# Optimization experiments

Measured on AMD Instinct MI355X. Metric: run time of the kernel, lower is better.

Reference implementation:

```python
import jax, jax.numpy as jnp
import numpy as np

B, N, D, H, O = 8, 2048, 64, 64, 64
ALPHA = 2.0  # LeakyReLU negative slope per module default
NEG = -9e15


def _lin(x, W, b):
    # torch nn.Linear: y = x @ W.T + b, W is [out, in]
    return x @ W.T + b


def setup_inputs() -> dict:
    key = jax.random.key(0)
    ks = jax.random.split(key, 32)
    f32 = jnp.float32
    x = jax.random.normal(ks[0], (B, N, D), f32)
    adj = jax.random.randint(ks[1], (B, N, N), 0, 2).astype(f32)
    c = jax.random.normal(ks[2], (B, N, H), f32)
    h = jax.random.normal(ks[3], (B, N, H), f32)
    s = 0.1
    W = jax.random.normal(ks[4], (D, H), f32) * s           # GAT weight
    a = jax.random.normal(ks[5], (2 * H, 1), f32) * s       # GAT attention vector
    def lin(k, out_d, in_d):
        k1, k2 = jax.random.split(k)
        return (jax.random.normal(k1, (out_d, in_d), f32) * s,
                jax.random.normal(k2, (out_d,), f32) * s)
    Wf, bWf = lin(ks[6], H, H); Wi, bWi = lin(ks[7], H, H)
    Wo, bWo = lin(ks[8], H, H); Wc, bWc = lin(ks[9], H, H)
    Uf, bUf = lin(ks[10], H, D); Ui, bUi = lin(ks[11], H, D)
    Uo, bUo = lin(ks[12], H, D); Uc, bUc = lin(ks[13], H, D)
    Wout, bout = lin(ks[14], O, 2 * H)
    return dict(x=x, adj=adj, c=c, h=h, W=W, a=a,
                Wf=Wf, bWf=bWf, Wi=Wi, bWi=bWi, Wo=Wo, bWo=bWo, Wc=Wc, bWc=bWc,
                Uf=Uf, bUf=bUf, Ui=Ui, bUi=bUi, Uo=Uo, bUo=bUo, Uc=Uc, bUc=bUc,
                Wout=Wout, bout=bout)


def reference(x, adj, c, h, W, a,
              Wf, bWf, Wi, bWi, Wo, bWo, Wc, bWc,
              Uf, bUf, Ui, bUi, Uo, bUo, Uc, bUc,
              Wout, bout):
    # ---- GraphAttentionLayer (eval mode: dropout is identity) ----
    Wh = x @ W                                   # [B,N,H]
    # e[b,i,j] = leakyrelu(a[:H].Wh_i + a[H:].Wh_j) -- same math as the
    a_src = (Wh @ a[:H]).squeeze(-1)             # [B,N]
    a_dst = (Wh @ a[H:]).squeeze(-1)             # [B,N]
    e = jax.nn.leaky_relu(a_src[:, :, None] + a_dst[:, None, :], ALPHA)  # [B,N,N]
    att = jnp.where(adj > 0, e, NEG)
    att = jax.nn.softmax(att, axis=2)
    x_hidden = jax.nn.elu(att @ Wh)              # [B,N,H] (concat=True)
    # ---- LSTMLayer step ----
    f_t = jax.nn.sigmoid(_lin(h, Wf, bWf) + _lin(x, Uf, bUf))
    i_t = jax.nn.sigmoid(_lin(h, Wi, bWi) + _lin(x, Ui, bUi))
    o_t = jax.nn.sigmoid(_lin(h, Wo, bWo) + _lin(x, Uo, bUo))
    c_hat = jnp.tanh(_lin(h, Wc, bWc) + _lin(x, Uc, bUc))
    c_t = f_t * c + i_t * c_hat
    h_t = o_t * jax.nn.relu(c_t)                 # gate = nn.ReLU() default
    total = jnp.concatenate([x_hidden, h_t], axis=2)  # [B,N,2H]
    output = jax.nn.relu(_lin(total, Wout, bout))     # [B,N,O]
    return (output, h_t, c_t)
```

## Files before the change

### kernel.cpp

```cpp
#include <hip/hip_runtime.h>
#include <math.h>

#define B_ 8
#define N_ 2048
#define NT_ (B_*N_)
#define OUTSZ (NT_*64)

#define WS_ASRC  0
#define WS_ADST  (WS_ASRC + NT_)
#define WS_WT    (WS_ADST + NT_)
#define WS_BB    (WS_WT + 128*256)
#define WS_WOT   (WS_BB + 256)
#define WS_PD    (WS_WOT + 128*64)
#define WS_PN    (WS_PD + 8*NT_)

typedef float f32x4 __attribute__((ext_vector_type(4)));
typedef __bf16 bf16x8 __attribute__((ext_vector_type(8)));
typedef __bf16 bf16x4 __attribute__((ext_vector_type(4)));

__device__ __forceinline__ float lrelu2(float x) { return x > 0.f ? x : 2.f * x; }
__device__ __forceinline__ float f4get(const float4& v, int k) { return k==0?v.x:(k==1?v.y:(k==2?v.z:v.w)); }

__global__ __launch_bounds__(256) void k1_wh(const float* __restrict__ x, const float* __restrict__ W,
                                             const float* __restrict__ a, float* __restrict__ ws,
                                             __bf16* __restrict__ whT,
                                             const float* Wf, const float* Wi, const float* Wo, const float* Wc,
                                             const float* Uf, const float* Ui, const float* Uo, const float* Uc,
                                             const float* bWf, const float* bWi, const float* bWo, const float* bWc,
                                             const float* bUf, const float* bUi, const float* bUo, const float* bUc,
                                             const float* Wout)
{
    __shared__ float xl[64 * 68];
    __shared__ float Wl[64 * 68];
    int t = threadIdx.x;
    if (blockIdx.x >= 256) {
        int idx = (blockIdx.x - 256) * 256 + t;
        if (idx < 128 * 256) {
            int k = idx >> 8, o = idx & 255;
            int g = o >> 6, u = o & 63;
            const float* Wg = (g == 0) ? Wf : (g == 1) ? Wi : (g == 2) ? Wo : Wc;
            const float* Ug = (g == 0) ? Uf : (g == 1) ? Ui : (g == 2) ? Uo : Uc;
            ws[WS_WT + idx] = (k < 64) ? Wg[u * 64 + k] : Ug[u * 64 + (k - 64)];
        } else if (idx < 128 * 256 + 256) {
            int o = idx - 128 * 256;
            int g = o >> 6, u = o & 63;
            const float* bW = (g == 0) ? bWf : (g == 1) ? bWi : (g == 2) ? bWo : bWc;
            const float* bU = (g == 0) ? bUf : (g == 1) ? bUi : (g == 2) ? bUo : bUc;
            ws[WS_BB + o] = bW[u] + bU[u];
        } else if (idx < 128 * 256 + 256 + 128 * 64) {
            int j = idx - (128 * 256 + 256);
            int k = j >> 6, u = j & 63;
            ws[WS_WOT + j] = Wout[u * 128 + k];
        }
        return;
    }
    int i0 = blockIdx.x * 64;
    #pragma unroll
    for (int it = 0; it < 4; ++it) {
        int f = t + 256 * it;
        int r = f >> 4, q = f & 15;
        *(float4*)&xl[r * 68 + q * 4] = *(const float4*)&x[i0 * 64 + f * 4];
        *(float4*)&Wl[r * 68 + q * 4] = *(const float4*)&W[f * 4];
    }
    __syncthreads();
    int cg = t & 15, rg = t >> 4;
    int c0 = cg * 4, r0 = rg * 4;
    float acc[4][4] = {};
    #pragma unroll
    for (int d0 = 0; d0 < 64; d0 += 4) {
        float4 wv[4], xv[4];
        #pragma unroll
        for (int k = 0; k < 4; ++k) wv[k] = *(float4*)&Wl[(d0 + k) * 68 + c0];
        #pragma unroll
        for (int ri = 0; ri < 4; ++ri) xv[ri] = *(float4*)&xl[(r0 + ri) * 68 + d0];
        #pragma unroll
        for (int ri = 0; ri < 4; ++ri)
            #pragma unroll
            for (int k = 0; k < 4; ++k) {
                float xs = f4get(xv[ri], k);
                acc[ri][0] += xs * wv[k].x; acc[ri][1] += xs * wv[k].y;
                acc[ri][2] += xs * wv[k].z; acc[ri][3] += xs * wv[k].w;
            }
    }
    int b = i0 >> 11;
    int rowb0 = (i0 & 2047) + r0;
    #pragma unroll
    for (int cj = 0; cj < 4; ++cj) {
        bf16x4 v;
        v[0] = (__bf16)acc[0][cj]; v[1] = (__bf16)acc[1][cj];
        v[2] = (__bf16)acc[2][cj]; v[3] = (__bf16)acc[3][cj];
        *(bf16x4*)&whT[((size_t)(b * 64 + c0 + cj)) * N_ + rowb0] = v;
    }
    float4 a0 = *(const float4*)&a[c0];
    float4 a1 = *(const float4*)&a[64 + c0];
    #pragma unroll
    for (int ri = 0; ri < 4; ++ri) {
        int row = i0 + r0 + ri;
        float s0 = acc[ri][0]*a0.x + acc[ri][1]*a0.y + acc[ri][2]*a0.z + acc[ri][3]*a0.w;
        float s1 = acc[ri][0]*a1.x + acc[ri][1]*a1.y + acc[ri][2]*a1.z + acc[ri][3]*a1.w;
        #pragma unroll
        for (int m = 1; m < 16; m <<= 1) { s0 += __shfl_xor(s0, m, 64); s1 += __shfl_xor(s1, m, 64); }
        if (cg == 0) { ws[WS_ASRC + row] = s0; ws[WS_ADST + row] = s1; }
    }
}

__global__ __launch_bounds__(256) void k2v10(const float* __restrict__ adj,
                                             const __bf16* __restrict__ whT,
                                             float* __restrict__ ws)
{
    __shared__ __bf16 adjt[2][16][268];
    __shared__ float lsa[4][16][68];
    __shared__ float lsd[4][16];
    __shared__ float gred[4];
    int tid = threadIdx.x;
    int lane = tid & 63, w = tid >> 6;
    int r = lane & 15, g = lane >> 4;
    int jr = blockIdx.x & 7;
    int rslab = blockIdx.x >> 3;
    int b = rslab >> 4;
    int row_base = rslab * 128;
    int jbeg = jr * 256 + w * 64;

    {
        float gm = -3.0e38f;
        for (int i = tid; i < N_; i += 256) gm = fmaxf(gm, ws[WS_ADST + b * N_ + i]);
        #pragma unroll
        for (int m_ = 1; m_ < 64; m_ <<= 1) gm = fmaxf(gm, __shfl_xor(gm, m_, 64));
        if (lane == 0) gred[w] = gm;
    }
    __syncthreads();
    float gmax = fmaxf(fmaxf(gred[0], gred[1]), fmaxf(gred[2], gred[3]));

    bf16x8 bfr[2][4];
    #pragma unroll
    for (int ks = 0; ks < 2; ++ks)
        #pragma unroll
        for (int n = 0; n < 4; ++n)
            bfr[ks][n] = *(const bf16x8*)&whT[(size_t)(b * 64 + n * 16 + r) * N_ + jbeg + ks * 32 + g * 8];
    float ejr[2][8];
    #pragma unroll
    for (int ks = 0; ks < 2; ++ks) {
        float4 d0 = *(const float4*)&ws[WS_ADST + b * N_ + jbeg + ks * 32 + g * 8];
        float4 d1 = *(const float4*)&ws[WS_ADST + b * N_ + jbeg + ks * 32 + g * 8 + 4];
        ejr[ks][0]=__expf(d0.x); ejr[ks][1]=__expf(d0.y); ejr[ks][2]=__expf(d0.z); ejr[ks][3]=__expf(d0.w);
        ejr[ks][4]=__expf(d1.x); ejr[ks][5]=__expf(d1.y); ejr[ks][6]=__expf(d1.z); ejr[ks][7]=__expf(d1.w);
    }
    float asv8[8];
    #pragma unroll
    for (int tt = 0; tt < 8; ++tt)
        asv8[tt] = ws[WS_ASRC + row_base + tt * 16 + r];

    f32x4 sreg[2][4];

#define SLOAD(T, S)                                                                        \
    {                                                                                      \
        _Pragma("unroll")                                                                  \
        for (int i = 0; i < 4; ++i)                                                        \
            sreg[S][i] = *(const f32x4*)&adj[(size_t)(row_base + (T) * 16 + w * 4 + i) * N_ \
                                             + jr * 256 + lane * 4];                       \
    }
#define SWRITE(T, S)                                                                       \
    {                                                                                      \
        _Pragma("unroll")                                                                  \
        for (int i = 0; i < 4; ++i) {                                                      \
            bf16x4 bv;                                                                     \
            bv[0] = (__bf16)sreg[S][i][0]; bv[1] = (__bf16)sreg[S][i][1];                  \
            bv[2] = (__bf16)sreg[S][i][2]; bv[3] = (__bf16)sreg[S][i][3];                  \
            *(bf16x4*)&adjt[(T) & 1][w * 4 + i][lane * 4] = bv;                            \
        }                                                                                  \
    }

    SLOAD(0, 0);
    SWRITE(0, 0);
    SLOAD(1, 1);
    asm volatile("s_waitcnt lgkmcnt(0)" ::: "memory");
    __builtin_amdgcn_s_barrier();
    asm volatile("" ::: "memory");

    #pragma unroll
    for (int t = 0; t < 8; ++t) {
        const int s = t & 1;
        if (t + 2 < 8) { SLOAD(t + 2, s); }
        float as = asv8[t];
        float M  = lrelu2(as + gmax);
        float c1 = __expf(as - M);
        float c2 = __expf(2.f * as - M);
        float thr = __expf(-as);
        f32x4 acc[4] = {{0.f,0.f,0.f,0.f},{0.f,0.f,0.f,0.f},{0.f,0.f,0.f,0.f},{0.f,0.f,0.f,0.f}};
        float dsum = 0.f;
        #pragma unroll
        for (int ks = 0; ks < 2; ++ks) {
            bf16x8 at = *(const bf16x8*)&adjt[s][r][w * 64 + ks * 32 + g * 8];
            bf16x8 af;
            float ds_ = 0.f;
            #pragma unroll
            for (int e = 0; e < 8; ++e) {
                float avv = (float)at[e];
                float E = ejr[ks][e];
                float p = (E > thr) ? c1 * E : (c2 * E) * E;
                p = (avv > 0.f) ? p : 0.f;
                ds_ += p;
                af[e] = (__bf16)p;
            }
            dsum += ds_;
            #pragma unroll
            for (int n = 0; n < 4; ++n)
                acc[n] = __builtin_amdgcn_mfma_f32_16x16x32_bf16(af, bfr[ks][n], acc[n], 0, 0, 0);
        }
        dsum += __shfl_xor(dsum, 16, 64);
        dsum += __shfl_xor(dsum, 32, 64);
        #pragma unroll
        for (int n = 0; n < 4; ++n)
            #pragma unroll
            for (int i = 0; i < 4; ++i)
                lsa[w][g * 4 + i][n * 16 + r] = acc[n][i];
        if (g == 0) lsd[w][r] = dsum;
        if (t + 1 < 8) { SWRITE(t + 1, s ^ 1); }
        asm volatile("s_waitcnt lgkmcnt(0)" ::: "memory");
        __builtin_amdgcn_s_barrier();
        asm volatile("" ::: "memory");
        {
            int rl = tid >> 4, h0 = (tid & 15) * 4;
            float4 sv = make_float4(0.f, 0.f, 0.f, 0.f);
            #pragma unroll
            for (int w2 = 0; w2 < 4; ++w2) {
                float4 q = *(const float4*)&lsa[w2][rl][h0];
                sv.x += q.x; sv.y += q.y; sv.z += q.z; sv.w += q.w;
            }
            int row0 = row_base + t * 16;
            *(float4*)&ws[WS_PN + ((size_t)jr * NT_ + row0 + rl) * 64 + h0] = sv;
            if (tid < 16)
                ws[WS_PD + jr * NT_ + row0 + tid] =
                    lsd[0][tid] + lsd[1][tid] + lsd[2][tid] + lsd[3][tid];
        }
        asm volatile("s_waitcnt lgkmcnt(0)" ::: "memory");
        __builtin_amdgcn_s_barrier();
        asm volatile("" ::: "memory");
    }
#undef SLOAD
#undef SWRITE
}

__global__ __launch_bounds__(256) void k3_lstm(const float* __restrict__ x, const float* __restrict__ c,
                                               const float* __restrict__ h, const float* __restrict__ ws,
                                               float* __restrict__ out)
{
    __shared__ float Al[16 * 132];
    __shared__ float gl[16 * 260];
    int t = threadIdx.x;
    int base = blockIdx.x * 16;
    {
        int r = t >> 4, k0 = (t & 15) * 8;
        const float* src = (k0 < 64) ? &h[(base + r) * 64 + k0] : &x[(base + r) * 64 + (k0 - 64)];
        *(float4*)&Al[r * 132 + k0]     = *(const float4*)&src[0];
        *(float4*)&Al[r * 132 + k0 + 4] = *(const float4*)&src[4];
    }
    __syncthreads();
    int og = t & 63, rg = t >> 6;
    int o0 = og * 4;
    const float* WT = &ws[WS_WT];
    float acc[4][4] = {};
    #pragma unroll
    for (int k0 = 0; k0 < 128; k0 += 4) {
        float4 wv[4], av[4];
        #pragma unroll
        for (int kk = 0; kk < 4; ++kk) wv[kk] = *(const float4*)&WT[(k0 + kk) * 256 + o0];
        #pragma unroll
        for (int rr = 0; rr < 4; ++rr) av[rr] = *(float4*)&Al[(rg + 4 * rr) * 132 + k0];
        #pragma unroll
        for (int rr = 0; rr < 4; ++rr)
            #pragma unroll
            for (int kk = 0; kk < 4; ++kk) {
                float as = f4get(av[rr], kk);
                acc[rr][0] += as * wv[kk].x; acc[rr][1] += as * wv[kk].y;
                acc[rr][2] += as * wv[kk].z; acc[rr][3] += as * wv[kk].w;
            }
    }
    float4 bbv = *(const float4*)&ws[WS_BB + o0];
    #pragma unroll
    for (int rr = 0; rr < 4; ++rr) {
        int r = rg + 4 * rr;
        *(float4*)&gl[r * 260 + o0] = make_float4(acc[rr][0] + bbv.x, acc[rr][1] + bbv.y,
                                                  acc[rr][2] + bbv.z, acc[rr][3] + bbv.w);
    }
    __syncthreads();
    int u = t & 63, rq = t >> 6;
    #pragma unroll
    for (int pp = 0; pp < 4; ++pp) {
        int r = rq + 4 * pp;
        float gf = gl[r * 260 + u];
        float gi = gl[r * 260 + 64 + u];
        float go = gl[r * 260 + 128 + u];
        float gc = gl[r * 260 + 192 + u];
        float fg = 1.f / (1.f + __expf(-gf));
        float ig = 1.f / (1.f + __expf(-gi));
        float oo = 1.f / (1.f + __expf(-go));
        float ch = tanhf(gc);
        float cv = c[(base + r) * 64 + u];
        float ct = fg * cv + ig * ch;
        float ht = oo * fmaxf(ct, 0.f);
        out[OUTSZ + (base + r) * 64 + u] = ht;
        out[2 * OUTSZ + (base + r) * 64 + u] = ct;
    }
}

__global__ __launch_bounds__(256) void k5_out(const float* __restrict__ ws, const float* __restrict__ bout,
                                              float* __restrict__ out)
{
    __shared__ float Al[64 * 132];
    int t = threadIdx.x;
    int base = blockIdx.x * 64;
    const float* ht = &out[OUTSZ];
    #pragma unroll
    for (int it = 0; it < 8; ++it) {
        int f = t + 256 * it;
        int r = f >> 5, q = f & 31;
        int k0 = q * 4;
        int row = base + r;
        float4 v;
        if (k0 < 64) {
            float4 s = make_float4(0.f, 0.f, 0.f, 0.f);
            float d = 0.f;
            #pragma unroll
            for (int jr = 0; jr < 8; ++jr) {
                float4 p = *(const float4*)&ws[WS_PN + ((size_t)jr * NT_ + row) * 64 + k0];
                s.x += p.x; s.y += p.y; s.z += p.z; s.w += p.w;
                d += ws[WS_PD + jr * NT_ + row];
            }
            float inv = 1.f / d;
            v.x = s.x * inv; v.x = v.x > 0.f ? v.x : expm1f(v.x);
            v.y = s.y * inv; v.y = v.y > 0.f ? v.y : expm1f(v.y);
            v.z = s.z * inv; v.z = v.z > 0.f ? v.z : expm1f(v.z);
            v.w = s.w * inv; v.w = v.w > 0.f ? v.w : expm1f(v.w);
        } else {
            v = *(const float4*)&ht[(size_t)row * 64 + (k0 - 64)];
        }
        *(float4*)&Al[r * 132 + k0] = v;
    }
    __syncthreads();
    int cg = t & 15, rgG = t >> 4;
    int c0 = cg * 4, r0 = rgG * 4;
    const float* WT = &ws[WS_WOT];
    float acc[4][4] = {};
    #pragma unroll
    for (int k0 = 0; k0 < 128; k0 += 4) {
        float4 wv[4], av[4];
        #pragma unroll
        for (int kk = 0; kk < 4; ++kk) wv[kk] = *(const float4*)&WT[(k0 + kk) * 64 + c0];
        #pragma unroll
        for (int ri = 0; ri < 4; ++ri) av[ri] = *(float4*)&Al[(r0 + ri) * 132 + k0];
        #pragma unroll
        for (int ri = 0; ri < 4; ++ri)
            #pragma unroll
            for (int kk = 0; kk < 4; ++kk) {
                float as = f4get(av[ri], kk);
                acc[ri][0] += as * wv[kk].x; acc[ri][1] += as * wv[kk].y;
                acc[ri][2] += as * wv[kk].z; acc[ri][3] += as * wv[kk].w;
            }
    }
    float4 bo = *(const float4*)&bout[c0];
    #pragma unroll
    for (int ri = 0; ri < 4; ++ri) {
        int row = base + r0 + ri;
        float4 o;
        o.x = fmaxf(acc[ri][0] + bo.x, 0.f);
        o.y = fmaxf(acc[ri][1] + bo.y, 0.f);
        o.z = fmaxf(acc[ri][2] + bo.z, 0.f);
        o.w = fmaxf(acc[ri][3] + bo.w, 0.f);
        *(float4*)&out[row * 64 + c0] = o;
    }
}

extern "C" void kernel_launch(void* const* d_in, const int* in_sizes, int n_in,
                              void* d_out, int out_size, void* d_ws, size_t ws_size,
                              hipStream_t stream)
{
    const float* x    = (const float*)d_in[0];
    const float* adj  = (const float*)d_in[1];
    const float* c    = (const float*)d_in[2];
    const float* h    = (const float*)d_in[3];
    const float* W    = (const float*)d_in[4];
    const float* a    = (const float*)d_in[5];
    const float* Wf   = (const float*)d_in[6];
    const float* bWf  = (const float*)d_in[7];
    const float* Wi   = (const float*)d_in[8];
    const float* bWi  = (const float*)d_in[9];
    const float* Wo   = (const float*)d_in[10];
    const float* bWo  = (const float*)d_in[11];
    const float* Wc   = (const float*)d_in[12];
    const float* bWc  = (const float*)d_in[13];
    const float* Uf   = (const float*)d_in[14];
    const float* bUf  = (const float*)d_in[15];
    const float* Ui   = (const float*)d_in[16];
    const float* bUi  = (const float*)d_in[17];
    const float* Uo   = (const float*)d_in[18];
    const float* bUo  = (const float*)d_in[19];
    const float* Uc   = (const float*)d_in[20];
    const float* bUc  = (const float*)d_in[21];
    const float* Wout = (const float*)d_in[22];
    const float* bout = (const float*)d_in[23];
    float* out = (float*)d_out;
    float* ws  = (float*)d_ws;
    __bf16* whT = (__bf16*)out;


    k1_wh<<<417, 256, 0, stream>>>(x, W, a, ws, whT,
                                   Wf, Wi, Wo, Wc, Uf, Ui, Uo, Uc,
                                   bWf, bWi, bWo, bWc, bUf, bUi, bUo, bUc, Wout);
    k3_lstm<<<NT_ / 16, 256, 0, stream>>>(x, c, h, ws, out);
    k2v10<<<1024, 256, 0, stream>>>(adj, whT, ws);
    k5_out<<<NT_ / 64, 256, 0, stream>>>(ws, bout, out);
}
```

Baseline: 86.47 us.

## Pack adjacency into bitmask in a separate kernel and simplify output GEMM tiling

Measured after the change: 97.36 us. 1.13x slower.

```diff
diff --git a/kernel.cpp b/kernel.cpp
--- a/kernel.cpp
+++ b/kernel.cpp
@@ -13,6 +13,7 @@
 #define WS_WOT   (WS_BB + 256)
 #define WS_PD    (WS_WOT + 128*64)
 #define WS_PN    (WS_PD + 8*NT_)
+#define WS_MASK  (WS_PN + 8*NT_*64)
 
 typedef float f32x4 __attribute__((ext_vector_type(4)));
 typedef __bf16 bf16x8 __attribute__((ext_vector_type(8)));
@@ -20,6 +21,22 @@
 
 __device__ __forceinline__ float lrelu2(float x) { return x > 0.f ? x : 2.f * x; }
 __device__ __forceinline__ float f4get(const float4& v, int k) { return k==0?v.x:(k==1?v.y:(k==2?v.z:v.w)); }
+
+__global__ __launch_bounds__(256) void kpack(const float* __restrict__ adj, unsigned* __restrict__ mask)
+{
+    size_t base = ((size_t)blockIdx.x * 256 + threadIdx.x) * 32;
+    const float* p = adj + base;
+    unsigned bits = 0u;
+    #pragma unroll
+    for (int q = 0; q < 8; ++q) {
+        float4 v = *(const float4*)&p[q * 4];
+        bits |= (v.x > 0.f ? 1u : 0u) << (q * 4);
+        bits |= (v.y > 0.f ? 1u : 0u) << (q * 4 + 1);
+        bits |= (v.z > 0.f ? 1u : 0u) << (q * 4 + 2);
+        bits |= (v.w > 0.f ? 1u : 0u) << (q * 4 + 3);
+    }
+    mask[base >> 5] = bits;
+}
 
 __global__ __launch_bounds__(256) void k1_wh(const float* __restrict__ x, const float* __restrict__ W,
                                              const float* __restrict__ a, float* __restrict__ ws,
@@ -104,11 +121,10 @@
     }
 }
 
-__global__ __launch_bounds__(256) void k2v10(const float* __restrict__ adj,
+__global__ __launch_bounds__(256) void k2v12(const unsigned* __restrict__ mask,
                                              const __bf16* __restrict__ whT,
                                              float* __restrict__ ws)
 {
-    __shared__ __bf16 adjt[2][16][268];
     __shared__ float lsa[4][16][68];
     __shared__ float lsd[4][16];
     __shared__ float gred[4];
@@ -120,6 +136,7 @@
     int b = rslab >> 4;
     int row_base = rslab * 128;
     int jbeg = jr * 256 + w * 64;
+    int jw0 = jr * 8 + w * 2;
 
     {
         float gm = -3.0e38f;
@@ -150,37 +167,16 @@
     for (int tt = 0; tt < 8; ++tt)
         asv8[tt] = ws[WS_ASRC + row_base + tt * 16 + r];
 
-    f32x4 sreg[2][4];
-
-#define SLOAD(T, S)                                                                        \
-    {                                                                                      \
-        _Pragma("unroll")                                                                  \
-        for (int i = 0; i < 4; ++i)                                                        \
-            sreg[S][i] = *(const f32x4*)&adj[(size_t)(row_base + (T) * 16 + w * 4 + i) * N_ \
-                                             + jr * 256 + lane * 4];                       \
-    }
-#define SWRITE(T, S)                                                                       \
-    {                                                                                      \
-        _Pragma("unroll")                                                                  \
-        for (int i = 0; i < 4; ++i) {                                                      \
-            bf16x4 bv;                                                                     \
-            bv[0] = (__bf16)sreg[S][i][0]; bv[1] = (__bf16)sreg[S][i][1];                  \
-            bv[2] = (__bf16)sreg[S][i][2]; bv[3] = (__bf16)sreg[S][i][3];                  \
-            *(bf16x4*)&adjt[(T) & 1][w * 4 + i][lane * 4] = bv;                            \
-        }                                                                                  \
-    }
-
-    SLOAD(0, 0);
-    SWRITE(0, 0);
-    SLOAD(1, 1);
-    asm volatile("s_waitcnt lgkmcnt(0)" ::: "memory");
-    __builtin_amdgcn_s_barrier();
-    asm volatile("" ::: "memory");
+    uint2 mreg[3];
+#define MLOAD(T, S)  mreg[S] = *(const uint2*)&mask[(size_t)(row_base + (T) * 16 + r) * 64 + jw0];
+
+    MLOAD(0, 0);
+    MLOAD(1, 1);
 
     #pragma unroll
     for (int t = 0; t < 8; ++t) {
-        const int s = t & 1;
-        if (t + 2 < 8) { SLOAD(t + 2, s); }
+        const int s = t % 3;
+        if (t + 2 < 8) { MLOAD(t + 2, (t + 2) % 3); }
         float as = asv8[t];
         float M  = lrelu2(as + gmax);
         float c1 = __expf(as - M);
@@ -190,15 +186,15 @@
         float dsum = 0.f;
         #pragma unroll
         for (int ks = 0; ks < 2; ++ks) {
-            bf16x8 at = *(const bf16x8*)&adjt[s][r][w * 64 + ks * 32 + g * 8];
+            unsigned word = ks ? mreg[s].y : mreg[s].x;
+            unsigned m8 = (word >> (g * 8)) & 0xffu;
             bf16x8 af;
             float ds_ = 0.f;
             #pragma unroll
             for (int e = 0; e < 8; ++e) {
-                float avv = (float)at[e];
                 float E = ejr[ks][e];
                 float p = (E > thr) ? c1 * E : (c2 * E) * E;
-                p = (avv > 0.f) ? p : 0.f;
+                p = ((m8 >> e) & 1u) ? p : 0.f;
                 ds_ += p;
                 af[e] = (__bf16)p;
             }
@@ -215,7 +211,6 @@
             for (int i = 0; i < 4; ++i)
                 lsa[w][g * 4 + i][n * 16 + r] = acc[n][i];
         if (g == 0) lsd[w][r] = dsum;
-        if (t + 1 < 8) { SWRITE(t + 1, s ^ 1); }
         asm volatile("s_waitcnt lgkmcnt(0)" ::: "memory");
         __builtin_amdgcn_s_barrier();
         asm volatile("" ::: "memory");
@@ -237,8 +232,7 @@
         __builtin_amdgcn_s_barrier();
         asm volatile("" ::: "memory");
     }
-#undef SLOAD
-#undef SWRITE
+#undef MLOAD
 }
 
 __global__ __launch_bounds__(256) void k3_lstm(const float* __restrict__ x, const float* __restrict__ c,
@@ -304,15 +298,15 @@
     }
 }
 
-__global__ __launch_bounds__(256) void k5_out(const float* __restrict__ ws, const float* __restrict__ bout,
-                                              float* __restrict__ out)
-{
-    __shared__ float Al[64 * 132];
+__global__ __launch_bounds__(256) void k5b(const float* __restrict__ ws, const float* __restrict__ bout,
+                                           float* __restrict__ out)
+{
+    __shared__ float Al[16 * 132];
     int t = threadIdx.x;
-    int base = blockIdx.x * 64;
+    int base = blockIdx.x * 16;
     const float* ht = &out[OUTSZ];
     #pragma unroll
-    for (int it = 0; it < 8; ++it) {
+    for (int it = 0; it < 2; ++it) {
         int f = t + 256 * it;
         int r = f >> 5, q = f & 31;
         int k0 = q * 4;
@@ -338,37 +332,23 @@
         *(float4*)&Al[r * 132 + k0] = v;
     }
     __syncthreads();
-    int cg = t & 15, rgG = t >> 4;
-    int c0 = cg * 4, r0 = rgG * 4;
+    int row = t >> 4, cg = t & 15;
+    int o0 = cg * 4;
     const float* WT = &ws[WS_WOT];
-    float acc[4][4] = {};
-    #pragma unroll
-    for (int k0 = 0; k0 < 128; k0 += 4) {
-        float4 wv[4], av[4];
-        #pragma unroll
-        for (int kk = 0; kk < 4; ++kk) wv[kk] = *(const float4*)&WT[(k0 + kk) * 64 + c0];
-        #pragma unroll
-        for (int ri = 0; ri < 4; ++ri) av[ri] = *(float4*)&Al[(r0 + ri) * 132 + k0];
-        #pragma unroll
-        for (int ri = 0; ri < 4; ++ri)
-            #pragma unroll
-            for (int kk = 0; kk < 4; ++kk) {
-                float as = f4get(av[ri], kk);
-                acc[ri][0] += as * wv[kk].x; acc[ri][1] += as * wv[kk].y;
-                acc[ri][2] += as * wv[kk].z; acc[ri][3] += as * wv[kk].w;
-            }
-    }
-    float4 bo = *(const float4*)&bout[c0];
-    #pragma unroll
-    for (int ri = 0; ri < 4; ++ri) {
-        int row = base + r0 + ri;
-        float4 o;
-        o.x = fmaxf(acc[ri][0] + bo.x, 0.f);
-        o.y = fmaxf(acc[ri][1] + bo.y, 0.f);
-        o.z = fmaxf(acc[ri][2] + bo.z, 0.f);
-        o.w = fmaxf(acc[ri][3] + bo.w, 0.f);
-        *(float4*)&out[row * 64 + c0] = o;
-    }
+    float4 acc = make_float4(0.f, 0.f, 0.f, 0.f);
+    #pragma unroll 8
+    for (int k = 0; k < 128; ++k) {
+        float a = Al[row * 132 + k];
+        float4 wv = *(const float4*)&WT[k * 64 + o0];
+        acc.x += a * wv.x; acc.y += a * wv.y; acc.z += a * wv.z; acc.w += a * wv.w;
+    }
+    float4 bo = *(const float4*)&bout[o0];
+    float4 o;
+    o.x = fmaxf(acc.x + bo.x, 0.f);
+    o.y = fmaxf(acc.y + bo.y, 0.f);
+    o.z = fmaxf(acc.z + bo.z, 0.f);
+    o.w = fmaxf(acc.w + bo.w, 0.f);
+    *(float4*)&out[(size_t)(base + row) * 64 + o0] = o;
 }
 
 extern "C" void kernel_launch(void* const* d_in, const int* in_sizes, int n_in,
@@ -402,12 +382,13 @@
     float* out = (float*)d_out;
     float* ws  = (float*)d_ws;
     __bf16* whT = (__bf16*)out;
-
-
+    unsigned* mask = (unsigned*)&ws[WS_MASK];
+
+    kpack<<<NT_ * (N_ / 32) / 256, 256, 0, stream>>>(adj, mask);
     k1_wh<<<417, 256, 0, stream>>>(x, W, a, ws, whT,
                                    Wf, Wi, Wo, Wc, Uf, Ui, Uo, Uc,
                                    bWf, bWi, bWo, bWc, bUf, bUi, bUo, bUc, Wout);
     k3_lstm<<<NT_ / 16, 256, 0, stream>>>(x, c, h, ws, out);
-    k2v10<<<1024, 256, 0, stream>>>(adj, whT, ws);
-    k5_out<<<NT_ / 64, 256, 0, stream>>>(ws, bout, out);
-}
+    k2v12<<<1024, 256, 0, stream>>>(mask, whT, ws);
+    k5b<<<NT_ / 16, 256, 0, stream>>>(ws, bout, out);
+}
```
